# Optimization experiments

Hardware: AMD Instinct MI355X
Metric: run time of the kernel (lower is better)

The kernel has to match this reference:

```python
import jax, jax.numpy as jnp
import numpy as np

V = 50000; C0 = 2000; C1 = 10000   # vocab and adaptive-softmax cutoffs
E = 512; H = 1024; B = 32; T = 128
H1 = H // 4; H2 = H // 16           # div_val = 4.0 per source formula
S1 = C1 - C0; S2 = V - C1


def setup_inputs() -> dict:
    key = jax.random.key(0)
    ks = jax.random.split(key, 12)
    # lengths sorted descending, max length == T (required by output.view(b*(T-1),-1))
    lengths = jnp.sort(jax.random.randint(ks[0], (B,), T // 2, T + 1))[::-1]
    lengths = lengths.at[0].set(T).astype(jnp.int64)
    x = jax.random.randint(ks[1], (B, T), 1, V)
    x = jnp.where(jnp.arange(T)[None, :] < lengths[:, None], x, 0).astype(jnp.int64)  # PAD=0 beyond length
    emb = (jax.random.normal(ks[2], (V, E), jnp.float32) * 0.02).at[0].set(0.0)  # padding_idx=0
    w_ih = jax.random.normal(ks[3], (3 * H, E), jnp.float32) * 0.02
    w_hh = jax.random.normal(ks[4], (3 * H, H), jnp.float32) * 0.02
    b_ih = jnp.zeros((3 * H,), jnp.float32)
    b_hh = jnp.zeros((3 * H,), jnp.float32)
    head_w = jax.random.normal(ks[5], (C0 + 2, H), jnp.float32) * 0.02   # shortlist + 2 cluster logits
    p1 = jax.random.normal(ks[6], (H1, H), jnp.float32) * 0.02
    t1 = jax.random.normal(ks[7], (S1, H1), jnp.float32) * 0.02
    p2 = jax.random.normal(ks[8], (H2, H), jnp.float32) * 0.02
    t2 = jax.random.normal(ks[9], (S2, H2), jnp.float32) * 0.02
    hidden = jnp.zeros((1, B, H), jnp.float32)
    return dict(x=x, lengths=lengths, hidden=hidden, emb=emb, w_ih=w_ih, w_hh=w_hh,
                b_ih=b_ih, b_hh=b_hh, head_w=head_w, p1=p1, t1=t1, p2=p2, t2=t2)


def gru_masked(inp, h0, w_ih, w_hh, b_ih, b_hh, lengths):
    """Torch GRU on packed sequence of lengths-1: frozen hidden + zero outputs past length."""
    xp = jnp.einsum('bte,ge->btg', inp, w_ih) + b_ih  # [B, T-1, 3H] input projections

    def step(h, args):
        xpt, t = args
        hp = h @ w_hh.T + b_hh
        xr, xz, xn = jnp.split(xpt, 3, axis=-1)
        hr, hz, hn = jnp.split(hp, 3, axis=-1)
        r = jax.nn.sigmoid(xr + hr)
        z = jax.nn.sigmoid(xz + hz)
        n = jnp.tanh(xn + r * hn)
        h_new = (1.0 - z) * n + z * h
        valid = (t < lengths - 1)[:, None]
        h = jnp.where(valid, h_new, h)          # freeze hidden past sequence end
        y = jnp.where(valid, h, 0.0)            # pad_packed_sequence zero-fills
        return h, y

    steps = jnp.arange(inp.shape[1])
    hT, ys = jax.lax.scan(step, h0, (jnp.swapaxes(xp, 0, 1), steps))
    return jnp.swapaxes(ys, 0, 1), hT  # [B, T-1, H], [B, H]


def adaptive_loss(out, targets, head_w, p1, t1, p2, t2):
    """AdaptiveLogSoftmaxWithLoss: mean NLL over shortlist + 2 tail clusters."""
    N = out.shape[0]
    head_lp = jax.nn.log_softmax(out @ head_w.T, axis=-1)  # [N, C0+2]
    idx = jnp.arange(N)
    lp_short = head_lp[idx, jnp.clip(targets, 0, C0 - 1)]

    def cluster_lp(p, t, ci, lo, size):
        tail_lp = jax.nn.log_softmax((out @ p.T) @ t.T, axis=-1)  # [N, size]
        rel = jnp.clip(targets - lo, 0, size - 1)
        return head_lp[:, C0 + ci] + tail_lp[idx, rel]

    lp1 = cluster_lp(p1, t1, 0, C0, S1)
    lp2 = cluster_lp(p2, t2, 1, C1, S2)
    logp = jnp.where(targets < C0, lp_short, jnp.where(targets < C1, lp1, lp2))
    return -jnp.mean(logp)


def reference(x, lengths, hidden, emb, w_ih, w_hh, b_ih, b_hh, head_w, p1, t1, p2, t2):
    inp = emb[x][:, :T - 1]  # dropout=0.0 -> identity
    ys, hT = gru_masked(inp, hidden[0], w_ih, w_hh, b_ih, b_hh, lengths)
    out = ys.reshape(B * (T - 1), H)
    targets = x[:, 1:].reshape(-1)
    loss = adaptive_loss(out, targets, head_w, p1, t1, p2, t2)
    return loss, hT[None]
```

## Files before the change

### kernel.cpp

```cpp
#include <hip/hip_runtime.h>
#include <math.h>

#define VV   50000
#define CC0  2000
#define CC1  10000
#define ED   512
#define HD   1024
#define BBATCH 32
#define TT   128
#define HH1  256
#define HH2  64
#define SS1  8000
#define SS2  40000
#define NR   4064
#define G3   3072

#define OFF_XP   0ull
#define OFF_YSB  12484608ull
#define OFF_HB   14565376ull
#define OFF_HT   14598144ull
#define OFF_P1B  14630912ull
#define OFF_P2B  15151104ull
#define OFF_WHB  15281152ull
#define OFF_T1B  16306176ull
#define OFF_PP1  17330176ull
#define OFF_PP2  17461248ull
#define OFF_SUM  17494016ull
#define OFF_LOSS (OFF_SUM + 6ull*4064ull)
#define OFF_INT  (OFF_LOSS + 64ull)
#define OFF_WIHB (OFF_INT + 8ull*4064ull)

#define ZERO_N (6*4064 + 64)
#define NBG 64
#define NCONS 192
#define NTILES 608

typedef __attribute__((ext_vector_type(8))) __bf16 bf16x8;
typedef __attribute__((ext_vector_type(4))) float f32x4;
typedef __attribute__((ext_vector_type(4))) unsigned int u32x4;
typedef unsigned long long u64;
typedef unsigned short u16;
struct ull2s { u64 x, y; };

__device__ __forceinline__ u16 f2bf(float f) {
    unsigned u = __builtin_bit_cast(unsigned, f);
    u += 0x7fff + ((u >> 16) & 1);
    return (u16)(u >> 16);
}

__global__ void init_k(const float* __restrict__ hidden, u16* __restrict__ hb0,
                       float* __restrict__ zreg, int* __restrict__ cnt1,
                       int* __restrict__ cnt2, int* __restrict__ bar)
{
    int i = blockIdx.x * 256 + threadIdx.x;
    if (i < BBATCH * HD) hb0[i] = f2bf(hidden[i]);
    int zi = i - BBATCH * HD;
    if (zi >= 0 && zi < ZERO_N) zreg[zi] = 0.f;
    if (zi == ZERO_N) { *cnt1 = 0; *cnt2 = 0; }
    int bi = zi - (ZERO_N + 1);
    if (bi >= 0 && bi < 2048) bar[bi] = 0;
}

__global__ void prep_k(const int* __restrict__ x, int* __restrict__ targets,
                       int* __restrict__ hselc, int* __restrict__ list1,
                       int* __restrict__ list2, int* __restrict__ cnt1, int* __restrict__ cnt2)
{
    int n = blockIdx.x * 256 + threadIdx.x;
    if (n >= NR) return;
    int t = n >> 5, b = n & 31;
    int tgt = x[b * TT + t + 1];
    targets[n] = tgt;
    hselc[n] = (tgt < CC0) ? tgt : ((tgt < CC1) ? CC0 : CC0 + 1);
    if (tgt >= CC0 && tgt < CC1) list1[atomicAdd(cnt1, 1)] = n;
    else if (tgt >= CC1)         list2[atomicAdd(cnt2, 1)] = n;
}

__global__ void cvt_bf16_k(const float* __restrict__ src, u16* __restrict__ dst, int n4)
{
    int i = blockIdx.x * 256 + threadIdx.x;
    if (i >= n4) return;
    float4 f = *(const float4*)(src + 4 * (size_t)i);
    union { u16 h[4]; u64 v; } u;
    u.h[0] = f2bf(f.x); u.h[1] = f2bf(f.y); u.h[2] = f2bf(f.z); u.h[3] = f2bf(f.w);
    *(u64*)&dst[4 * (size_t)i] = u.v;
}

__global__ void cvt_multi_k(const float* __restrict__ s0, u16* __restrict__ d0, int n0,
                            const float* __restrict__ s1, u16* __restrict__ d1, int n1,
                            const float* __restrict__ s2, u16* __restrict__ d2, int n2,
                            const float* __restrict__ s3, u16* __restrict__ d3, int n3,
                            const float* __restrict__ s4, u16* __restrict__ d4, int n4)
{
    int i = blockIdx.x * 256 + threadIdx.x;
    const float* s; u16* d; int off = i;
    if (off < n0) { s = s0; d = d0; }
    else if ((off -= n0) < n1) { s = s1; d = d1; }
    else if ((off -= n1) < n2) { s = s2; d = d2; }
    else if ((off -= n2) < n3) { s = s3; d = d3; }
    else if ((off -= n3) < n4) { s = s4; d = d4; }
    else return;
    float4 f = *(const float4*)(s + 4 * (size_t)off);
    union { u16 h[4]; u64 v; } u;
    u.h[0] = f2bf(f.x); u.h[1] = f2bf(f.y); u.h[2] = f2bf(f.z); u.h[3] = f2bf(f.w);
    *(u64*)&d[4 * (size_t)off] = u.v;
}

__global__ void emb_gather_k(const int* __restrict__ x, const float* __restrict__ emb,
                             u16* __restrict__ embA)
{
    int idx = blockIdx.x * 256 + threadIdx.x;
    if (idx >= NR * 64) return;
    int n = idx >> 6;
    int kk = (idx & 63) << 3;
    int b = n & 31, t = n >> 5;
    int tok = x[b * TT + t];
    const float* ap = emb + (size_t)tok * ED + kk;
    float4 f0 = *(const float4*)ap;
    float4 f1 = *(const float4*)(ap + 4);
    union { u16 h[8]; u32x4 v; } u;
    u.h[0] = f2bf(f0.x); u.h[1] = f2bf(f0.y); u.h[2] = f2bf(f0.z); u.h[3] = f2bf(f0.w);
    u.h[4] = f2bf(f1.x); u.h[5] = f2bf(f1.y); u.h[6] = f2bf(f1.z); u.h[7] = f2bf(f1.w);
    *(u32x4*)&embA[(size_t)n * ED + kk] = u.v;
}

template<int EPI, int BFP32>
__global__ void __launch_bounds__(256)
mfma_gemm_k(const u16* __restrict__ Ab, const void* __restrict__ Bsrc,
            int Mdirect, int N, int K,
            const int* __restrict__ rowmap, const int* __restrict__ cntp,
            u16* __restrict__ outB, int ldo,
            float* __restrict__ gsum, float* __restrict__ gsel,
            const int* __restrict__ selcol, const int* __restrict__ targets, int lo)
{
    const int M = cntp ? *cntp : Mdirect;
    const int rbase = blockIdx.x * 128;
    if (rbase >= M) return;
    const int cbase = blockIdx.y * 128;

    __shared__ u16 As[128 * 40];
    __shared__ u16 Bs[128 * 40];
    __shared__ const u16* aptr[128];
    __shared__ int rown[128];
    __shared__ float redl[128 * 2];

    const int tid = threadIdx.x;
    if (tid < 128) {
        int rid = -1;
        if (rbase + tid < M) rid = rowmap ? rowmap[rbase + tid] : (rbase + tid);
        rown[tid] = rid;
        aptr[tid] = (rid >= 0) ? (Ab + (size_t)rid * K) : nullptr;
    }
    __syncthreads();

    const int lane = tid & 63, wid = tid >> 6;
    const int n16 = lane & 15, quad = lane >> 4;
    const int m0 = (wid >> 1) * 64, n0 = (wid & 1) * 64;
    const int i = tid >> 1, half = tid & 1;

    f32x4 acc[4][4];
#pragma unroll
    for (int a = 0; a < 4; a++)
#pragma unroll
        for (int b = 0; b < 4; b++) acc[a][b] = (f32x4){0.f, 0.f, 0.f, 0.f};

    for (int k0 = 0; k0 < K; k0 += 32) {
        const u16* ap = aptr[i];
        u32x4 a0 = {0,0,0,0}, a1 = a0;
        if (ap) {
            a0 = *(const u32x4*)(ap + k0 + half * 16);
            a1 = *(const u32x4*)(ap + k0 + half * 16 + 8);
        }
        u32x4 b0 = {0,0,0,0}, b1 = b0;
        int c = cbase + i;
        if (c < N) {
            if (BFP32) {
                const float* bp = (const float*)Bsrc + (size_t)c * K + k0 + half * 16;
                float4 f0 = *(const float4*)(bp);
                float4 f1 = *(const float4*)(bp + 4);
                float4 f2 = *(const float4*)(bp + 8);
                float4 f3 = *(const float4*)(bp + 12);
                union { u16 h[16]; u32x4 v[2]; } u;
                u.h[0]=f2bf(f0.x); u.h[1]=f2bf(f0.y); u.h[2]=f2bf(f0.z); u.h[3]=f2bf(f0.w);
                u.h[4]=f2bf(f1.x); u.h[5]=f2bf(f1.y); u.h[6]=f2bf(f1.z); u.h[7]=f2bf(f1.w);
                u.h[8]=f2bf(f2.x); u.h[9]=f2bf(f2.y); u.h[10]=f2bf(f2.z); u.h[11]=f2bf(f2.w);
                u.h[12]=f2bf(f3.x); u.h[13]=f2bf(f3.y); u.h[14]=f2bf(f3.z); u.h[15]=f2bf(f3.w);
                b0 = u.v[0]; b1 = u.v[1];
            } else {
                const u16* bp = (const u16*)Bsrc + (size_t)c * K + k0 + half * 16;
                b0 = *(const u32x4*)(bp);
                b1 = *(const u32x4*)(bp + 8);
            }
        }
        __syncthreads();
        *(u32x4*)&As[i * 40 + half * 16]     = a0;
        *(u32x4*)&As[i * 40 + half * 16 + 8] = a1;
        *(u32x4*)&Bs[i * 40 + half * 16]     = b0;
        *(u32x4*)&Bs[i * 40 + half * 16 + 8] = b1;
        __syncthreads();

        bf16x8 av[4], bv[4];
#pragma unroll
        for (int mi = 0; mi < 4; mi++)
            av[mi] = *(const bf16x8*)&As[(m0 + mi * 16 + n16) * 40 + quad * 8];
#pragma unroll
        for (int ni = 0; ni < 4; ni++)
            bv[ni] = *(const bf16x8*)&Bs[(n0 + ni * 16 + n16) * 40 + quad * 8];
#pragma unroll
        for (int mi = 0; mi < 4; mi++)
#pragma unroll
            for (int ni = 0; ni < 4; ni++)
                acc[mi][ni] = __builtin_amdgcn_mfma_f32_16x16x32_bf16(
                    av[mi], bv[ni], acc[mi][ni], 0, 0, 0);
    }

    __syncthreads();
    if (EPI == 0) {
#pragma unroll
        for (int mi = 0; mi < 4; mi++)
#pragma unroll
            for (int ni = 0; ni < 4; ni++)
#pragma unroll
                for (int r = 0; r < 4; r++) {
                    int row = rbase + m0 + mi * 16 + quad * 4 + r;
                    int col = cbase + n0 + ni * 16 + n16;
                    if (row < M && col < N)
                        outB[(size_t)row * ldo + col] = f2bf(acc[mi][ni][r]);
                }
    } else if (EPI == 3) {
#pragma unroll
        for (int mi = 0; mi < 4; mi++)
#pragma unroll
            for (int ni = 0; ni < 4; ni++)
#pragma unroll
                for (int r = 0; r < 4; r++) {
                    int row = rbase + m0 + mi * 16 + quad * 4 + r;
                    int col = cbase + n0 + ni * 16 + n16;
                    if (row < M && col < N)
                        gsum[(size_t)row * ldo + col] = acc[mi][ni][r] + gsel[col];
                }
    } else {
#pragma unroll
        for (int mi = 0; mi < 4; mi++)
#pragma unroll
            for (int r = 0; r < 4; r++) {
                int lrow = m0 + mi * 16 + quad * 4 + r;
                int nid = rown[lrow];
                float s = 0.f;
                if (nid >= 0) {
                    int sc = (EPI == 1) ? selcol[nid] : (targets[nid] - lo);
#pragma unroll
                    for (int ni = 0; ni < 4; ni++) {
                        int col = cbase + n0 + ni * 16 + n16;
                        if (col < N) {
                            float v = acc[mi][ni][r];
                            s += __expf(v);
                            if (col == sc) gsel[nid] = v;
                        }
                    }
                }
                s += __shfl_xor(s, 1);
                s += __shfl_xor(s, 2);
                s += __shfl_xor(s, 4);
                s += __shfl_xor(s, 8);
                if (n16 == 0) redl[lrow * 2 + (wid & 1)] = s;
            }
        __syncthreads();
        if (tid < 128) {
            int nid = rown[tid];
            if (nid >= 0) atomicAdd(&gsum[nid], redl[tid * 2] + redl[tid * 2 + 1]);
        }
    }
}

__global__ void __launch_bounds__(256, 1)
gru_fused_k(const float* __restrict__ xp, const float* __restrict__ hidden,
            u16* __restrict__ hb0, u16* __restrict__ hb1,
            const float* __restrict__ w_hh, const float* __restrict__ b_hh,
            const int* __restrict__ lengths, u16* __restrict__ ys,
            float* __restrict__ hT, int* __restrict__ flags,
            const u16* __restrict__ whb, const u16* __restrict__ pp1b,
            const u16* __restrict__ pp2b, u16* __restrict__ p1b,
            u16* __restrict__ p2b, float* __restrict__ hsum,
            float* __restrict__ hsel, const int* __restrict__ hselc)
{
    __shared__ u16 Blds[48 * 1032];
    __shared__ u16 As[128 * 40];
    __shared__ u16 Bs[128 * 40];
    __shared__ const u16* aptr[128];
    __shared__ int rown[128];
    __shared__ float redl[128 * 2];

    const int tid = threadIdx.x;
    const int lane = tid & 63;
    const int n16 = lane & 15, quad = lane >> 4;

    if (blockIdx.x < NBG) {
        const int bid = blockIdx.x;
        const int j0 = bid * 16;
        const int wid = tid >> 6;

        for (int idx = tid; idx < 48 * 1024; idx += 256) {
            int r = idx >> 10, k = idx & 1023;
            int g = r >> 4, c = r & 15;
            Blds[r * 1032 + k] = f2bf(w_hh[(size_t)(g * HD + j0 + c) * HD + k]);
        }

        const int col = j0 + n16;
        float bh0 = 0.f, bh1 = 0.f, bh2 = 0.f;
        float hold[4];
        int len[4] = {0, 0, 0, 0};
        if (tid < 128) {
            bh0 = b_hh[col]; bh1 = b_hh[HD + col]; bh2 = b_hh[2 * HD + col];
#pragma unroll
            for (int r = 0; r < 4; r++) {
                int b = wid * 16 + quad * 4 + r;
                len[r] = lengths[b];
                hold[r] = hidden[b * HD + col];
            }
        }
        __syncthreads();

        const int boff = n16 * 1032 + quad * 8;
        const size_t rowoff = (size_t)(wid * 16 + n16) * HD + quad * 8;

        for (int t = 0; t < TT - 1; t++) {
            if (tid < 128) {
                const u16* hb = (t & 1) ? hb1 : hb0;
                u16* hbn = (t & 1) ? hb0 : hb1;

                float xrv[4], xzv[4], xnv[4];
#pragma unroll
                for (int r = 0; r < 4; r++) {
                    int b = wid * 16 + quad * 4 + r;
                    const float* xpt = xp + ((size_t)t * BBATCH + b) * G3 + col;
                    xrv[r] = xpt[0]; xzv[r] = xpt[HD]; xnv[r] = xpt[2 * HD];
                }

                const u16* arow = hb + rowoff;
                u64 apf[64];
#pragma unroll
                for (int ks = 0; ks < 32; ks++) {
                    apf[2*ks]   = __hip_atomic_load((const u64*)(arow + ks*32),
                                      __ATOMIC_RELAXED, __HIP_MEMORY_SCOPE_AGENT);
                    apf[2*ks+1] = __hip_atomic_load((const u64*)(arow + ks*32 + 4),
                                      __ATOMIC_RELAXED, __HIP_MEMORY_SCOPE_AGENT);
                }

                f32x4 acc0 = {0.f, 0.f, 0.f, 0.f}, acc1 = acc0, acc2 = acc0;
#pragma unroll
                for (int ks = 0; ks < 32; ks++) {
                    ull2s av2; av2.x = apf[2*ks]; av2.y = apf[2*ks+1];
                    bf16x8 av = __builtin_bit_cast(bf16x8, av2);
                    bf16x8 b0 = *(const bf16x8*)&Blds[boff + ks*32];
                    bf16x8 b1 = *(const bf16x8*)&Blds[16*1032 + boff + ks*32];
                    bf16x8 b2 = *(const bf16x8*)&Blds[32*1032 + boff + ks*32];
                    acc0 = __builtin_amdgcn_mfma_f32_16x16x32_bf16(av, b0, acc0, 0, 0, 0);
                    acc1 = __builtin_amdgcn_mfma_f32_16x16x32_bf16(av, b1, acc1, 0, 0, 0);
                    acc2 = __builtin_amdgcn_mfma_f32_16x16x32_bf16(av, b2, acc2, 0, 0, 0);
                }

#pragma unroll
                for (int r = 0; r < 4; r++) {
                    int b = wid * 16 + quad * 4 + r;
                    float hr = acc0[r] + bh0, hz = acc1[r] + bh1, hn = acc2[r] + bh2;
                    float rg = 1.f / (1.f + __expf(-(xrv[r] + hr)));
                    float zg = 1.f / (1.f + __expf(-(xzv[r] + hz)));
                    float nv = tanhf(xnv[r] + rg * hn);
                    bool valid = t < (len[r] - 1);
                    float hnew = valid ? (1.f - zg) * nv + zg * hold[r] : hold[r];
                    hold[r] = hnew;
                    __hip_atomic_store(hbn + (size_t)b * HD + col, f2bf(hnew),
                                       __ATOMIC_RELAXED, __HIP_MEMORY_SCOPE_AGENT);
                    __hip_atomic_store(ys + ((size_t)t * BBATCH + b) * HD + col,
                                       f2bf(valid ? hnew : 0.f),
                                       __ATOMIC_RELAXED, __HIP_MEMORY_SCOPE_AGENT);
                    if (t == TT - 2) hT[b * HD + col] = hnew;
                }
            }

            __syncthreads();
            if (tid < 64) {
                if (tid == 0) {
                    __builtin_amdgcn_s_waitcnt(0);
                    __hip_atomic_store(&flags[bid * 32], t + 1, __ATOMIC_RELAXED,
                                       __HIP_MEMORY_SCOPE_AGENT);
                }
                int guard = 0;
                while (__hip_atomic_load(&flags[tid * 32], __ATOMIC_RELAXED,
                                         __HIP_MEMORY_SCOPE_AGENT) < t + 1
                       && guard < (1 << 20)) {
                    __builtin_amdgcn_s_sleep(1);
                    guard++;
                }
            }
            asm volatile("" ::: "memory");
            __syncthreads();
        }
    } else {
        const int wid4 = tid >> 6;
        const int m0 = (wid4 >> 1) * 64, n0 = (wid4 & 1) * 64;
        const int i = tid >> 1, half = tid & 1;
        const int cb = blockIdx.x - NBG;

        for (int g = cb; g < NTILES; g += NCONS) {
            int x, y, N, ldo = 0, epi;
            const u16* Bp; u16* outp = nullptr;
            if (g < 512)      { x = g >> 4;  y = g & 15; N = CC0 + 2; Bp = whb;  epi = 1; }
            else if (g < 576) { int gg = g - 512; x = gg >> 1; y = gg & 1;
                                N = HH1; Bp = pp1b; outp = p1b; ldo = HH1; epi = 0; }
            else              { x = g - 576; y = 0;
                                N = HH2; Bp = pp2b; outp = p2b; ldo = HH2; epi = 0; }
            const int rbase = x * 128, cbase = y * 128;

            int tneed = 4 * x + 4; if (tneed > TT - 1) tneed = TT - 1;
            {
                int guard = 0;
                while (true) {
                    int f = __hip_atomic_load(&flags[lane * 32], __ATOMIC_RELAXED,
                                              __HIP_MEMORY_SCOPE_AGENT);
                    if (__ballot(f >= tneed) == ~0ull) break;
                    if (++guard >= (1 << 20)) break;
                    __builtin_amdgcn_s_sleep(8);
                }
            }
            asm volatile("" ::: "memory");

            __syncthreads();
            if (tid < 128) {
                int rid = (rbase + tid < NR) ? (rbase + tid) : -1;
                rown[tid] = rid;
                aptr[tid] = (rid >= 0) ? (ys + (size_t)rid * HD) : nullptr;
            }
            __syncthreads();

            f32x4 acc[4][4];
#pragma unroll
            for (int a = 0; a < 4; a++)
#pragma unroll
                for (int b = 0; b < 4; b++) acc[a][b] = (f32x4){0.f, 0.f, 0.f, 0.f};

            for (int k0 = 0; k0 < HD; k0 += 32) {
                const u16* ap = aptr[i];
                u64 a0 = 0, a1 = 0, a2 = 0, a3 = 0;
                if (ap) {
                    const u64* p = (const u64*)(ap + k0 + half * 16);
                    a0 = __hip_atomic_load(p,     __ATOMIC_RELAXED, __HIP_MEMORY_SCOPE_AGENT);
                    a1 = __hip_atomic_load(p + 1, __ATOMIC_RELAXED, __HIP_MEMORY_SCOPE_AGENT);
                    a2 = __hip_atomic_load(p + 2, __ATOMIC_RELAXED, __HIP_MEMORY_SCOPE_AGENT);
                    a3 = __hip_atomic_load(p + 3, __ATOMIC_RELAXED, __HIP_MEMORY_SCOPE_AGENT);
                }
                u32x4 b0v = {0,0,0,0}, b1v = b0v;
                int c = cbase + i;
                if (c < N) {
                    const u16* bp = Bp + (size_t)c * HD + k0 + half * 16;
                    b0v = *(const u32x4*)(bp);
                    b1v = *(const u32x4*)(bp + 8);
                }
                __syncthreads();
                *(u64*)&As[i * 40 + half * 16]      = a0;
                *(u64*)&As[i * 40 + half * 16 + 4]  = a1;
                *(u64*)&As[i * 40 + half * 16 + 8]  = a2;
                *(u64*)&As[i * 40 + half * 16 + 12] = a3;
                *(u32x4*)&Bs[i * 40 + half * 16]     = b0v;
                *(u32x4*)&Bs[i * 40 + half * 16 + 8] = b1v;
                __syncthreads();

                bf16x8 av[4], bv[4];
#pragma unroll
                for (int mi = 0; mi < 4; mi++)
                    av[mi] = *(const bf16x8*)&As[(m0 + mi * 16 + n16) * 40 + quad * 8];
#pragma unroll
                for (int ni = 0; ni < 4; ni++)
                    bv[ni] = *(const bf16x8*)&Bs[(n0 + ni * 16 + n16) * 40 + quad * 8];
#pragma unroll
                for (int mi = 0; mi < 4; mi++)
#pragma unroll
                    for (int ni = 0; ni < 4; ni++)
                        acc[mi][ni] = __builtin_amdgcn_mfma_f32_16x16x32_bf16(
                            av[mi], bv[ni], acc[mi][ni], 0, 0, 0);
            }

            __syncthreads();
            if (epi == 0) {
#pragma unroll
                for (int mi = 0; mi < 4; mi++)
#pragma unroll
                    for (int ni = 0; ni < 4; ni++)
#pragma unroll
                        for (int r = 0; r < 4; r++) {
                            int row = rbase + m0 + mi * 16 + quad * 4 + r;
                            int col = cbase + n0 + ni * 16 + n16;
                            if (row < NR && col < N)
                                outp[(size_t)row * ldo + col] = f2bf(acc[mi][ni][r]);
                        }
            } else {
#pragma unroll
                for (int mi = 0; mi < 4; mi++)
#pragma unroll
                    for (int r = 0; r < 4; r++) {
                        int lrow = m0 + mi * 16 + quad * 4 + r;
                        int nid = rown[lrow];
                        float s = 0.f;
                        if (nid >= 0) {
                            int sc = hselc[nid];
#pragma unroll
                            for (int ni = 0; ni < 4; ni++) {
                                int col = cbase + n0 + ni * 16 + n16;
                                if (col < N) {
                                    float v = acc[mi][ni][r];
                                    s += __expf(v);
                                    if (col == sc) hsel[nid] = v;
                                }
                            }
                        }
                        s += __shfl_xor(s, 1);
                        s += __shfl_xor(s, 2);
                        s += __shfl_xor(s, 4);
                        s += __shfl_xor(s, 8);
                        if (n16 == 0) redl[lrow * 2 + (wid4 & 1)] = s;
                    }
                __syncthreads();
                if (tid < 128) {
                    int nid = rown[tid];
                    if (nid >= 0) atomicAdd(&hsum[nid], redl[tid * 2] + redl[tid * 2 + 1]);
                }
            }
        }
    }
}

__global__ void finish_k(const float* __restrict__ hsum, const float* __restrict__ hsel,
                         const float* __restrict__ t1sum, const float* __restrict__ t1sel,
                         const float* __restrict__ t2sum, const float* __restrict__ t2sel,
                         const int* __restrict__ targets, float* __restrict__ losssum)
{
    __shared__ float red[256];
    int n = blockIdx.x * 256 + threadIdx.x;
    float lp = 0.f;
    if (n < NR) {
        lp = hsel[n] - logf(hsum[n]);
        int tgt = targets[n];
        if (tgt >= CC1)      lp += t2sel[n] - logf(t2sum[n]);
        else if (tgt >= CC0) lp += t1sel[n] - logf(t1sum[n]);
    }
    red[threadIdx.x] = lp;
    __syncthreads();
    for (int s = 128; s > 0; s >>= 1) {
        if (threadIdx.x < s) red[threadIdx.x] += red[threadIdx.x + s];
        __syncthreads();
    }
    if (threadIdx.x == 0) atomicAdd(losssum, red[0]);
}

__global__ void out_k(const float* __restrict__ losssum, const float* __restrict__ hT,
                      float* __restrict__ out)
{
    int i = blockIdx.x * 256 + threadIdx.x;
    if (i == 0) out[0] = -losssum[0] / (float)NR;
    if (i < BBATCH * HD) out[1 + i] = hT[i];
}

extern "C" void kernel_launch(void* const* d_in, const int* in_sizes, int n_in,
                              void* d_out, int out_size, void* d_ws, size_t ws_size,
                              hipStream_t stream)
{
    const int*   x       = (const int*)d_in[0];
    const int*   lengths = (const int*)d_in[1];
    const float* hidden  = (const float*)d_in[2];
    const float* emb     = (const float*)d_in[3];
    const float* w_ih    = (const float*)d_in[4];
    const float* w_hh    = (const float*)d_in[5];
    const float* b_ih    = (const float*)d_in[6];
    const float* b_hh    = (const float*)d_in[7];
    const float* head_w  = (const float*)d_in[8];
    const float* p1      = (const float*)d_in[9];
    const float* t1      = (const float*)d_in[10];
    const float* p2      = (const float*)d_in[11];
    const float* t2      = (const float*)d_in[12];

    float* ws = (float*)d_ws;
    float* xp    = ws + OFF_XP;
    u16*   ysb   = (u16*)(ws + OFF_YSB);
    u16*   hb0   = (u16*)(ws + OFF_HB);
    u16*   hb1   = hb0 + BBATCH * HD;
    float* hT    = ws + OFF_HT;
    u16*   p1b   = (u16*)(ws + OFF_P1B);
    u16*   p2b   = (u16*)(ws + OFF_P2B);
    u16*   whb   = (u16*)(ws + OFF_WHB);
    u16*   t1b   = (u16*)(ws + OFF_T1B);
    u16*   pp1b  = (u16*)(ws + OFF_PP1);
    u16*   pp2b  = (u16*)(ws + OFF_PP2);
    float* hsum  = ws + OFF_SUM;
    float* hsel  = hsum + 4064;
    float* t1sum = hsel + 4064;
    float* t1sel = t1sum + 4064;
    float* t2sum = t1sel + 4064;
    float* t2sel = t2sum + 4064;
    float* losss = ws + OFF_LOSS;
    int* ib      = (int*)(ws + OFF_INT);
    int* targets = ib;
    int* hselc   = ib + 4064;
    int* list1   = ib + 2 * 4064;
    int* list2   = ib + 3 * 4064;
    int* cnt1    = ib + 4 * 4064;
    int* cnt2    = cnt1 + 1;
    int* flags   = ib + 5 * 4064;

    u16* embA = (u16*)(ws + OFF_YSB);
    u16* wihb = (u16*)(ws + OFF_WIHB);
    u16* t2b  = (u16*)(ws + OFF_XP);

    float* out = (float*)d_out;

    init_k<<<232, 256, 0, stream>>>(hidden, hb0, hsum, cnt1, cnt2, flags);
    prep_k<<<16, 256, 0, stream>>>(x, targets, hselc, list1, list2, cnt1, cnt2);

    cvt_multi_k<<<(1499648 + 255) / 256, 256, 0, stream>>>(
        w_ih, wihb, 393216,
        head_w, whb, 512512,
        t1, t1b, 512000,
        p1, pp1b, 65536,
        p2, pp2b, 16384);

    emb_gather_k<<<(NR * 64 + 255) / 256, 256, 0, stream>>>(x, emb, embA);
    mfma_gemm_k<3, 0><<<dim3(32, 24), 256, 0, stream>>>(
        embA, wihb, NR, G3, ED, nullptr, nullptr, nullptr, G3,
        xp, (float*)b_ih, nullptr, nullptr, 0);

    gru_fused_k<<<NBG + NCONS, 256, 0, stream>>>(
        xp, hidden, hb0, hb1, w_hh, b_hh, lengths, ysb, hT, flags,
        whb, pp1b, pp2b, p1b, p2b, hsum, hsel, hselc);

    cvt_bf16_k<<<(640000 + 255) / 256, 256, 0, stream>>>(t2, t2b, 640000);

    mfma_gemm_k<2, 0><<<dim3(32, 63), 256, 0, stream>>>(
        p1b, t1b, 0, SS1, HH1, list1, cnt1, nullptr, 0,
        t1sum, t1sel, nullptr, targets, CC0);
    mfma_gemm_k<2, 0><<<dim3(32, 313), 256, 0, stream>>>(
        p2b, t2b, 0, SS2, HH2, list2, cnt2, nullptr, 0,
        t2sum, t2sel, nullptr, targets, CC1);

    finish_k<<<16, 256, 0, stream>>>(hsum, hsel, t1sum, t1sel, t2sum, t2sel,
                                     targets, losss);
    out_k<<<128, 256, 0, stream>>>(losss, hT, out);
}
```

Measured before the change: 1.354 ms.

## Fold tail-cluster GEMMs into persistent GRU kernel with dynamic work queue

The two tail-cluster logit GEMMs move into the consumer blocks of the fused GRU kernel. Blocks now pull work from a global atomic counter that spans the head, projection and tail tiles. Tail tiles wait on per-row-tile completion counters set by the projection tiles, so tail work can run while the serial recurrence is still going. This removes the separate t2 conversion kernel and two GEMM launches; t2 is now converted from fp32 inside the load loop. In exchange, the row-compaction lists are dropped, so tail logits are computed for every row rather than only rows whose targets fall in each cluster, which costs extra compute, especially for cluster 1.

```diff
diff --git a/kernel.cpp b/kernel.cpp
--- a/kernel.cpp
+++ b/kernel.cpp
@@ -33,7 +33,13 @@
 #define ZERO_N (6*4064 + 64)
 #define NBG 64
 #define NCONS 192
-#define NTILES 608
+#define NBARZ 4160
+
+#define G_HEAD 512
+#define G_P1   576
+#define G_P2   608
+#define G_T1   2624
+#define G_TOT  12640
 
 typedef __attribute__((ext_vector_type(8))) __bf16 bf16x8;
 typedef __attribute__((ext_vector_type(4))) float f32x4;
@@ -49,21 +55,18 @@
 }
 
 __global__ void init_k(const float* __restrict__ hidden, u16* __restrict__ hb0,
-                       float* __restrict__ zreg, int* __restrict__ cnt1,
-                       int* __restrict__ cnt2, int* __restrict__ bar)
+                       float* __restrict__ zreg, int* __restrict__ bar)
 {
     int i = blockIdx.x * 256 + threadIdx.x;
     if (i < BBATCH * HD) hb0[i] = f2bf(hidden[i]);
     int zi = i - BBATCH * HD;
     if (zi >= 0 && zi < ZERO_N) zreg[zi] = 0.f;
-    if (zi == ZERO_N) { *cnt1 = 0; *cnt2 = 0; }
     int bi = zi - (ZERO_N + 1);
-    if (bi >= 0 && bi < 2048) bar[bi] = 0;
+    if (bi >= 0 && bi < NBARZ) bar[bi] = 0;
 }
 
 __global__ void prep_k(const int* __restrict__ x, int* __restrict__ targets,
-                       int* __restrict__ hselc, int* __restrict__ list1,
-                       int* __restrict__ list2, int* __restrict__ cnt1, int* __restrict__ cnt2)
+                       int* __restrict__ hselc)
 {
     int n = blockIdx.x * 256 + threadIdx.x;
     if (n >= NR) return;
@@ -71,18 +74,6 @@
     int tgt = x[b * TT + t + 1];
     targets[n] = tgt;
     hselc[n] = (tgt < CC0) ? tgt : ((tgt < CC1) ? CC0 : CC0 + 1);
-    if (tgt >= CC0 && tgt < CC1) list1[atomicAdd(cnt1, 1)] = n;
-    else if (tgt >= CC1)         list2[atomicAdd(cnt2, 1)] = n;
-}
-
-__global__ void cvt_bf16_k(const float* __restrict__ src, u16* __restrict__ dst, int n4)
-{
-    int i = blockIdx.x * 256 + threadIdx.x;
-    if (i >= n4) return;
-    float4 f = *(const float4*)(src + 4 * (size_t)i);
-    union { u16 h[4]; u64 v; } u;
-    u.h[0] = f2bf(f.x); u.h[1] = f2bf(f.y); u.h[2] = f2bf(f.z); u.h[3] = f2bf(f.w);
-    *(u64*)&dst[4 * (size_t)i] = u.v;
 }
 
 __global__ void cvt_multi_k(const float* __restrict__ s0, u16* __restrict__ d0, int n0,
@@ -214,19 +205,7 @@
     }
 
     __syncthreads();
-    if (EPI == 0) {
-#pragma unroll
-        for (int mi = 0; mi < 4; mi++)
-#pragma unroll
-            for (int ni = 0; ni < 4; ni++)
-#pragma unroll
-                for (int r = 0; r < 4; r++) {
-                    int row = rbase + m0 + mi * 16 + quad * 4 + r;
-                    int col = cbase + n0 + ni * 16 + n16;
-                    if (row < M && col < N)
-                        outB[(size_t)row * ldo + col] = f2bf(acc[mi][ni][r]);
-                }
-    } else if (EPI == 3) {
+    if (EPI == 3) {
 #pragma unroll
         for (int mi = 0; mi < 4; mi++)
 #pragma unroll
@@ -238,38 +217,8 @@
                     if (row < M && col < N)
                         gsum[(size_t)row * ldo + col] = acc[mi][ni][r] + gsel[col];
                 }
-    } else {
-#pragma unroll
-        for (int mi = 0; mi < 4; mi++)
-#pragma unroll
-            for (int r = 0; r < 4; r++) {
-                int lrow = m0 + mi * 16 + quad * 4 + r;
-                int nid = rown[lrow];
-                float s = 0.f;
-                if (nid >= 0) {
-                    int sc = (EPI == 1) ? selcol[nid] : (targets[nid] - lo);
-#pragma unroll
-                    for (int ni = 0; ni < 4; ni++) {
-                        int col = cbase + n0 + ni * 16 + n16;
-                        if (col < N) {
-                            float v = acc[mi][ni][r];
-                            s += __expf(v);
-                            if (col == sc) gsel[nid] = v;
-                        }
-                    }
-                }
-                s += __shfl_xor(s, 1);
-                s += __shfl_xor(s, 2);
-                s += __shfl_xor(s, 4);
-                s += __shfl_xor(s, 8);
-                if (n16 == 0) redl[lrow * 2 + (wid & 1)] = s;
-            }
-        __syncthreads();
-        if (tid < 128) {
-            int nid = rown[tid];
-            if (nid >= 0) atomicAdd(&gsum[nid], redl[tid * 2] + redl[tid * 2 + 1]);
-        }
     }
+    (void)redl; (void)selcol; (void)targets; (void)lo; (void)outB;
 }
 
 __global__ void __launch_bounds__(256, 1)
@@ -281,7 +230,11 @@
             const u16* __restrict__ whb, const u16* __restrict__ pp1b,
             const u16* __restrict__ pp2b, u16* __restrict__ p1b,
             u16* __restrict__ p2b, float* __restrict__ hsum,
-            float* __restrict__ hsel, const int* __restrict__ hselc)
+            float* __restrict__ hsel, const int* __restrict__ hselc,
+            const int* __restrict__ targets, const u16* __restrict__ t1b,
+            const float* __restrict__ t2f, float* __restrict__ t1sum,
+            float* __restrict__ t1sel, float* __restrict__ t2sum,
+            float* __restrict__ t2sel)
 {
     __shared__ u16 Blds[48 * 1032];
     __shared__ u16 As[128 * 40];
@@ -289,10 +242,15 @@
     __shared__ const u16* aptr[128];
     __shared__ int rown[128];
     __shared__ float redl[128 * 2];
+    __shared__ int g_sh;
 
     const int tid = threadIdx.x;
     const int lane = tid & 63;
     const int n16 = lane & 15, quad = lane >> 4;
+
+    int* pdone1  = flags + 2048;
+    int* pdone2  = flags + 2048 + 1024;
+    int* workctr = flags + 2048 + 2048;
 
     if (blockIdx.x < NBG) {
         const int bid = blockIdx.x;
@@ -400,36 +358,62 @@
         const int wid4 = tid >> 6;
         const int m0 = (wid4 >> 1) * 64, n0 = (wid4 & 1) * 64;
         const int i = tid >> 1, half = tid & 1;
-        const int cb = blockIdx.x - NBG;
-
-        for (int g = cb; g < NTILES; g += NCONS) {
-            int x, y, N, ldo = 0, epi;
-            const u16* Bp; u16* outp = nullptr;
-            if (g < 512)      { x = g >> 4;  y = g & 15; N = CC0 + 2; Bp = whb;  epi = 1; }
-            else if (g < 576) { int gg = g - 512; x = gg >> 1; y = gg & 1;
-                                N = HH1; Bp = pp1b; outp = p1b; ldo = HH1; epi = 0; }
-            else              { x = g - 576; y = 0;
-                                N = HH2; Bp = pp2b; outp = p2b; ldo = HH2; epi = 0; }
+
+        while (true) {
+            __syncthreads();
+            if (tid == 0) g_sh = atomicAdd(workctr, 1);
+            __syncthreads();
+            const int g = g_sh;
+            if (g >= G_TOT) break;
+
+            int x, y, N, K, type;
+            const u16* Ap; const void* Bp; int bfp32 = 0;
+            u16* outp = nullptr; int ldo = 0;
+            float *esum = nullptr, *esel = nullptr; int lo = 0, usehc = 0;
+            if (g < G_HEAD)      { type=0; x=g>>4; y=g&15; N=CC0+2; K=HD;
+                                   Ap=ys;  Bp=whb;  esum=hsum;  esel=hsel;  usehc=1; }
+            else if (g < G_P1)   { type=1; int j=g-G_HEAD; x=j>>1; y=j&1; N=HH1; K=HD;
+                                   Ap=ys;  Bp=pp1b; outp=p1b; ldo=HH1; }
+            else if (g < G_P2)   { type=2; x=g-G_P1; y=0; N=HH2; K=HD;
+                                   Ap=ys;  Bp=pp2b; outp=p2b; ldo=HH2; }
+            else if (g < G_T1)   { type=3; int j=g-G_P2; x=j/63;  y=j-x*63;  N=SS1; K=HH1;
+                                   Ap=p1b; Bp=t1b;  esum=t1sum; esel=t1sel; lo=CC0; }
+            else                 { type=4; int j=g-G_T1; x=j/313; y=j-x*313; N=SS2; K=HH2;
+                                   Ap=p2b; Bp=t2f;  bfp32=1; esum=t2sum; esel=t2sel; lo=CC1; }
             const int rbase = x * 128, cbase = y * 128;
 
-            int tneed = 4 * x + 4; if (tneed > TT - 1) tneed = TT - 1;
-            {
-                int guard = 0;
-                while (true) {
-                    int f = __hip_atomic_load(&flags[lane * 32], __ATOMIC_RELAXED,
-                                              __HIP_MEMORY_SCOPE_AGENT);
-                    if (__ballot(f >= tneed) == ~0ull) break;
-                    if (++guard >= (1 << 20)) break;
-                    __builtin_amdgcn_s_sleep(8);
+            if (type <= 2) {
+                int tneed = 4 * x + 4; if (tneed > TT - 1) tneed = TT - 1;
+                if (tid < 64) {
+                    int guard = 0;
+                    while (true) {
+                        int f = __hip_atomic_load(&flags[lane * 32], __ATOMIC_RELAXED,
+                                                  __HIP_MEMORY_SCOPE_AGENT);
+                        if (__ballot(f >= tneed) == ~0ull) break;
+                        if (++guard >= (1 << 20)) break;
+                        __builtin_amdgcn_s_sleep(32);
+                    }
+                }
+            } else {
+                if (tid == 0) {
+                    int* pd  = (type == 3) ? &pdone1[x * 32] : &pdone2[x * 32];
+                    int need = (type == 3) ? 2 : 1;
+                    int guard = 0;
+                    while (__hip_atomic_load(pd, __ATOMIC_RELAXED,
+                                             __HIP_MEMORY_SCOPE_AGENT) < need
+                           && guard < (1 << 20)) {
+                        __builtin_amdgcn_s_sleep(32);
+                        guard++;
+                    }
                 }
             }
             asm volatile("" ::: "memory");
-
             __syncthreads();
+
             if (tid < 128) {
                 int rid = (rbase + tid < NR) ? (rbase + tid) : -1;
                 rown[tid] = rid;
-                aptr[tid] = (rid >= 0) ? (ys + (size_t)rid * HD) : nullptr;
+                aptr[tid] = (rid >= 0) ? (Ap + (size_t)rid * K) : nullptr;
             }
             __syncthreads();
 
@@ -439,7 +423,7 @@
 #pragma unroll
                 for (int b = 0; b < 4; b++) acc[a][b] = (f32x4){0.f, 0.f, 0.f, 0.f};
 
-            for (int k0 = 0; k0 < HD; k0 += 32) {
+            for (int k0 = 0; k0 < K; k0 += 32) {
                 const u16* ap = aptr[i];
                 u64 a0 = 0, a1 = 0, a2 = 0, a3 = 0;
                 if (ap) {
@@ -452,9 +436,23 @@
                 u32x4 b0v = {0,0,0,0}, b1v = b0v;
                 int c = cbase + i;
                 if (c < N) {
-                    const u16* bp = Bp + (size_t)c * HD + k0 + half * 16;
-                    b0v = *(const u32x4*)(bp);
-                    b1v = *(const u32x4*)(bp + 8);
+                    if (bfp32) {
+                        const float* bp = (const float*)Bp + (size_t)c * K + k0 + half * 16;
+                        float4 f0 = *(const float4*)(bp);
+                        float4 f1 = *(const float4*)(bp + 4);
+                        float4 f2 = *(const float4*)(bp + 8);
+                        float4 f3 = *(const float4*)(bp + 12);
+                        union { u16 h[16]; u32x4 v[2]; } u;
+                        u.h[0]=f2bf(f0.x); u.h[1]=f2bf(f0.y); u.h[2]=f2bf(f0.z); u.h[3]=f2bf(f0.w);
+                        u.h[4]=f2bf(f1.x); u.h[5]=f2bf(f1.y); u.h[6]=f2bf(f1.z); u.h[7]=f2bf(f1.w);
+                        u.h[8]=f2bf(f2.x); u.h[9]=f2bf(f2.y); u.h[10]=f2bf(f2.z); u.h[11]=f2bf(f2.w);
+                        u.h[12]=f2bf(f3.x); u.h[13]=f2bf(f3.y); u.h[14]=f2bf(f3.z); u.h[15]=f2bf(f3.w);
+                        b0v = u.v[0]; b1v = u.v[1];
+                    } else {
+                        const u16* bp = (const u16*)Bp + (size_t)c * K + k0 + half * 16;
+                        b0v = *(const u32x4*)(bp);
+                        b1v = *(const u32x4*)(bp + 8);
+                    }
                 }
                 __syncthreads();
                 *(u64*)&As[i * 40 + half * 16]      = a0;
@@ -481,7 +479,7 @@
             }
 
             __syncthreads();
-            if (epi == 0) {
+            if (type == 1 || type == 2) {
 #pragma unroll
                 for (int mi = 0; mi < 4; mi++)
 #pragma unroll
@@ -491,8 +489,16 @@
                             int row = rbase + m0 + mi * 16 + quad * 4 + r;
                             int col = cbase + n0 + ni * 16 + n16;
                             if (row < NR && col < N)
-                                outp[(size_t)row * ldo + col] = f2bf(acc[mi][ni][r]);
+                                __hip_atomic_store(&outp[(size_t)row * ldo + col],
+                                                   f2bf(acc[mi][ni][r]),
+                                                   __ATOMIC_RELAXED, __HIP_MEMORY_SCOPE_AGENT);
                         }
+                __syncthreads();
+                if (tid == 0) {
+                    __builtin_amdgcn_s_waitcnt(0);
+                    __hip_atomic_fetch_add((type == 1) ? &pdone1[x * 32] : &pdone2[x * 32],
+                                           1, __ATOMIC_RELAXED, __HIP_MEMORY_SCOPE_AGENT);
+                }
             } else {
 #pragma unroll
                 for (int mi = 0; mi < 4; mi++)
@@ -502,14 +508,14 @@
                         int nid = rown[lrow];
                         float s = 0.f;
                         if (nid >= 0) {
-                            int sc = hselc[nid];
+                            int sc = usehc ? hselc[nid] : (targets[nid] - lo);
 #pragma unroll
                             for (int ni = 0; ni < 4; ni++) {
                                 int col = cbase + n0 + ni * 16 + n16;
                                 if (col < N) {
                                     float v = acc[mi][ni][r];
                                     s += __expf(v);
-                                    if (col == sc) hsel[nid] = v;
+                                    if (col == sc) esel[nid] = v;
                                 }
                             }
                         }
@@ -522,7 +528,7 @@
                 __syncthreads();
                 if (tid < 128) {
                     int nid = rown[tid];
-                    if (nid >= 0) atomicAdd(&hsum[nid], redl[tid * 2] + redl[tid * 2 + 1]);
+                    if (nid >= 0) atomicAdd(&esum[nid], redl[tid * 2] + redl[tid * 2 + 1]);
                 }
             }
         }
@@ -600,20 +606,15 @@
     int* ib      = (int*)(ws + OFF_INT);
     int* targets = ib;
     int* hselc   = ib + 4064;
-    int* list1   = ib + 2 * 4064;
-    int* list2   = ib + 3 * 4064;
-    int* cnt1    = ib + 4 * 4064;
-    int* cnt2    = cnt1 + 1;
     int* flags   = ib + 5 * 4064;
 
     u16* embA = (u16*)(ws + OFF_YSB);
     u16* wihb = (u16*)(ws + OFF_WIHB);
-    u16* t2b  = (u16*)(ws + OFF_XP);
 
     float* out = (float*)d_out;
 
-    init_k<<<232, 256, 0, stream>>>(hidden, hb0, hsum, cnt1, cnt2, flags);
-    prep_k<<<16, 256, 0, stream>>>(x, targets, hselc, list1, list2, cnt1, cnt2);
+    init_k<<<240, 256, 0, stream>>>(hidden, hb0, hsum, flags);
+    prep_k<<<16, 256, 0, stream>>>(x, targets, hselc);
 
     cvt_multi_k<<<(1499648 + 255) / 256, 256, 0, stream>>>(
         w_ih, wihb, 393216,
@@ -629,16 +630,8 @@
 
     gru_fused_k<<<NBG + NCONS, 256, 0, stream>>>(
         xp, hidden, hb0, hb1, w_hh, b_hh, lengths, ysb, hT, flags,
-        whb, pp1b, pp2b, p1b, p2b, hsum, hsel, hselc);
-
-    cvt_bf16_k<<<(640000 + 255) / 256, 256, 0, stream>>>(t2, t2b, 640000);
-
-    mfma_gemm_k<2, 0><<<dim3(32, 63), 256, 0, stream>>>(
-        p1b, t1b, 0, SS1, HH1, list1, cnt1, nullptr, 0,
-        t1sum, t1sel, nullptr, targets, CC0);
-    mfma_gemm_k<2, 0><<<dim3(32, 313), 256, 0, stream>>>(
-        p2b, t2b, 0, SS2, HH2, list2, cnt2, nullptr, 0,
-        t2sum, t2sel, nullptr, targets, CC1);
+        whb, pp1b, pp2b, p1b, p2b, hsum, hsel, hselc,
+        targets, t1b, t2, t1sum, t1sel, t2sum, t2sel);
 
     finish_k<<<16, 256, 0, stream>>>(hsum, hsel, t1sum, t1sel, t2sum, t2sel,
                                      targets, losss);
```

Measured after the change: 1.758 ms. 29.8% more time.
